# Kernel tuning notes

Hardware: AMD Instinct MI355X
Metric: run time of the kernel (lower is better)

The kernel has to match this reference:

```python
import jax, jax.numpy as jnp
import numpy as np
from jax.scipy.special import logsumexp

B, T, H, S = 32, 2000, 256, 63  # batch, time steps, hidden dim, num_states (=num_classes)


def setup_inputs() -> dict:
    key = jax.random.key(0)
    ks = jax.random.split(key, 5)
    return {
        "ctc_logits": jax.random.normal(ks[0], (B, T, S), dtype=jnp.float32),
        "frame_embeddings": jax.random.normal(ks[1], (B, T, H), dtype=jnp.float32),
        "keyword_tokens": jax.random.randint(ks[2], (B, 32), 0, S),
        "W1": jax.random.normal(ks[3], (2 * H, H), dtype=jnp.float32) * 0.02,
        "b1": jnp.zeros((H,), dtype=jnp.float32),
        "W2": jax.random.normal(ks[4], (H, S), dtype=jnp.float32) * 0.02,
        "b2": jnp.zeros((S,), dtype=jnp.float32),
    }


def reference(ctc_logits, frame_embeddings, keyword_tokens, W1, b1, W2, b2):
    Bv, Tv, Sv = ctc_logits.shape
    logp = jax.nn.log_softmax(ctc_logits, axis=-1)  # (B,T,S)

    # transition scores for frame pair (t, t-1) <-> trans_all[t-1], batched over all t at once
    pairs = jnp.concatenate([frame_embeddings[:, 1:], frame_embeddings[:, :-1]], axis=-1)  # (B,T-1,2H)
    h = jax.nn.relu(jnp.einsum("bti,ij->btj", pairs, W1) + b1)
    trans = jnp.einsum("bti,ij->btj", h, W2) + b2  # (B,T-1,S)

    lp_t = jnp.swapaxes(logp, 0, 1)   # (T,B,S)
    tr_t = jnp.swapaxes(trans, 0, 1)  # (T-1,B,S)

    # forward recursion
    f0 = jnp.zeros((Bv, Sv), dtype=logp.dtype).at[:, 0].set(
        logp[jnp.arange(Bv), 0, keyword_tokens[:, 0]])

    def fstep(f_prev, x):
        lp, tr = x  # each (B,S)
        # [b,j,s] = f_prev[b,j] + lp[b,s] + tr[b,s]; reduce over j (prev state)
        scores = f_prev[:, :, None] + lp[:, None, :] + tr[:, None, :]
        f = logsumexp(scores, axis=1)
        return f, f

    _, f_rest = jax.lax.scan(fstep, f0, (lp_t[1:], tr_t))
    fwd = jnp.concatenate([f0[None], f_rest], axis=0)  # (T,B,S)

    # backward recursion (reverse scan); backward at t uses pair (t+1, t) = trans[t]
    bT = jnp.zeros((Bv, Sv), dtype=logp.dtype)

    def bstep(b_next, x):
        lp, tr = x  # lp = logp[t+1], tr = trans[t]
        # [b,s,k] = b_next[b,k] + lp[b,s] + tr[b,s]; reduce over k (next state)
        scores = b_next[:, None, :] + lp[:, :, None] + tr[:, :, None]
        b = logsumexp(scores, axis=2)
        return b, b

    _, b_rest = jax.lax.scan(bstep, bT, (lp_t[1:], tr_t), reverse=True)
    bwd = jnp.concatenate([b_rest, bT[None]], axis=0)  # (T,B,S)

    alignments = jax.nn.softmax(jnp.swapaxes(fwd + bwd, 0, 1), axis=-1)  # (B,T,S)
    return alignments
```

## Files before the change

### kernel.cpp

```cpp
#include <hip/hip_runtime.h>
#include <stdint.h>

#define NB 32
#define NT 2000
#define NH 256
#define NS 63
#define LDSROW 264

typedef __attribute__((ext_vector_type(8))) short bf16x8;
typedef __attribute__((ext_vector_type(4))) float f32x4;

__device__ inline unsigned short f2bf(float f) {
  union { float f; uint32_t u; } v; v.f = f;
  return (unsigned short)((v.u + 0x7fffu + ((v.u >> 16) & 1u)) >> 16);
}
__device__ inline unsigned int pk2(float a, float b) {
  return (unsigned int)f2bf(a) | ((unsigned int)f2bf(b) << 16);
}
__device__ inline bf16x8 pack8(const float* g) {
  union { bf16x8 v; unsigned int u[4]; } c;
  c.u[0] = pk2(g[0], g[1]); c.u[1] = pk2(g[2], g[3]);
  c.u[2] = pk2(g[4], g[5]); c.u[3] = pk2(g[6], g[7]);
  return c.v;
}

#define NSLOT1 (16 * 4 * 4 * 64)
#define NSLOT2 (8 * 4 * 64)
#define WS_NEEDED ((size_t)(NSLOT1 + NSLOT2) * 16)

__global__ __launch_bounds__(256) void prep_weights(
    const float* __restrict__ W1, const float* __restrict__ W2,
    unsigned short* __restrict__ w1f, unsigned short* __restrict__ w2f) {
  const int tid = blockIdx.x * 256 + threadIdx.x;
  if (tid < NSLOT1) {
    const int lane = tid & 63;
    const int quad = lane >> 4, l16 = lane & 15;
    int r = tid >> 6;
    const int tn = r & 3; r >>= 2;
    const int wv = r & 3; r >>= 2;
    const int km = r;
    const int kb = (km >> 3) * 256 + (km & 7) * 32 + quad * 8;
    const int n = wv * 64 + tn * 16 + l16;
    ushort4 lo, hi;
    lo.x = f2bf(W1[(size_t)(kb + 0) * NH + n]);
    lo.y = f2bf(W1[(size_t)(kb + 1) * NH + n]);
    lo.z = f2bf(W1[(size_t)(kb + 2) * NH + n]);
    lo.w = f2bf(W1[(size_t)(kb + 3) * NH + n]);
    hi.x = f2bf(W1[(size_t)(kb + 4) * NH + n]);
    hi.y = f2bf(W1[(size_t)(kb + 5) * NH + n]);
    hi.z = f2bf(W1[(size_t)(kb + 6) * NH + n]);
    hi.w = f2bf(W1[(size_t)(kb + 7) * NH + n]);
    *(ushort4*)&w1f[(size_t)tid * 8] = lo;
    *(ushort4*)&w1f[(size_t)tid * 8 + 4] = hi;
  } else if (tid < NSLOT1 + NSLOT2) {
    const int t2 = tid - NSLOT1;
    const int lane = t2 & 63;
    const int quad = lane >> 4, l16 = lane & 15;
    const int tn = (t2 >> 6) & 3;
    const int ks = t2 >> 8;
    const int kb = ks * 32 + quad * 8;
    const int n = tn * 16 + l16;
    ushort4 lo = {0, 0, 0, 0}, hi = {0, 0, 0, 0};
    if (n < NS) {
      lo.x = f2bf(W2[(size_t)(kb + 0) * NS + n]);
      lo.y = f2bf(W2[(size_t)(kb + 1) * NS + n]);
      lo.z = f2bf(W2[(size_t)(kb + 2) * NS + n]);
      lo.w = f2bf(W2[(size_t)(kb + 3) * NS + n]);
      hi.x = f2bf(W2[(size_t)(kb + 4) * NS + n]);
      hi.y = f2bf(W2[(size_t)(kb + 5) * NS + n]);
      hi.z = f2bf(W2[(size_t)(kb + 6) * NS + n]);
      hi.w = f2bf(W2[(size_t)(kb + 7) * NS + n]);
    }
    *(ushort4*)&w2f[(size_t)t2 * 8] = lo;
    *(ushort4*)&w2f[(size_t)t2 * 8 + 4] = hi;
  }
}

template <bool PACKED>
__global__ __launch_bounds__(256, 4) void fused_kernel(
    const float* __restrict__ E, const float* __restrict__ logits,
    const int* __restrict__ kw,
    const float* __restrict__ W1, const float* __restrict__ W2,
    const unsigned short* __restrict__ w1f, const unsigned short* __restrict__ w2f,
    const float* __restrict__ b1, const float* __restrict__ b2,
    float* __restrict__ out) {
  const int b = blockIdx.y;
  const int a0 = blockIdx.x * 63;
  const int base = a0 - 1;
  const int tid = threadIdx.x;
  const int w = tid >> 6;
  const int lane = tid & 63;
  const int quad = lane >> 4;
  const int l16 = lane & 15;
  const int n0 = w * 64;

  __shared__ unsigned short lds[65 * LDSROW];
  float* TRf = (float*)lds;

  const float* Eb = E + (size_t)b * NT * NH;
  const float* lb = logits + (size_t)b * NT * NS;

  #pragma unroll
  for (int it = 0; it < 16; ++it) {
    const int row = it * 4 + w;
    int tr = base + row;
    tr = (tr < 0) ? 0 : (tr > NT - 1 ? NT - 1 : tr);
    float4 v = *(const float4*)&Eb[(size_t)tr * NH + (lane << 2)];
    ushort4 o;
    o.x = f2bf(v.x); o.y = f2bf(v.y); o.z = f2bf(v.z); o.w = f2bf(v.w);
    *(ushort4*)&lds[row * LDSROW + (lane << 2)] = o;
  }
  if (tid < 64) {
    int tr = base + 64; if (tr > NT - 1) tr = NT - 1;
    float4 v = *(const float4*)&Eb[(size_t)tr * NH + (lane << 2)];
    ushort4 o;
    o.x = f2bf(v.x); o.y = f2bf(v.y); o.z = f2bf(v.z); o.w = f2bf(v.w);
    *(ushort4*)&lds[64 * LDSROW + (lane << 2)] = o;
  }
  __syncthreads();

  f32x4 acc[4][4];
  #pragma unroll
  for (int tm = 0; tm < 4; ++tm)
    #pragma unroll
    for (int tn = 0; tn < 4; ++tn) acc[tm][tn] = (f32x4){0.f, 0.f, 0.f, 0.f};

  if constexpr (PACKED) {
    const unsigned short* wbase = w1f + (size_t)(((w << 2) * 64) + lane) * 8;
#define W1F_AT(KM, TN) \
  (*(const bf16x8*)(wbase + ((size_t)((((KM) << 4) + (TN))) << 9)))
    bf16x8 cb0 = W1F_AT(0, 0), cb1 = W1F_AT(0, 1);
    bf16x8 cb2 = W1F_AT(0, 2), cb3 = W1F_AT(0, 3);
    #pragma unroll
    for (int km = 0; km < 16; ++km) {
      bf16x8 nb0, nb1, nb2, nb3;
      if (km < 15) {
        nb0 = W1F_AT(km + 1, 0); nb1 = W1F_AT(km + 1, 1);
        nb2 = W1F_AT(km + 1, 2); nb3 = W1F_AT(km + 1, 3);
      }
      const int aoff = (km >> 3) ? 0 : 1;
      bf16x8 af[4];
      #pragma unroll
      for (int tm = 0; tm < 4; ++tm)
        af[tm] = *(const bf16x8*)&lds[(tm * 16 + l16 + aoff) * LDSROW +
                                      (km & 7) * 32 + quad * 8];
      #pragma unroll
      for (int tm = 0; tm < 4; ++tm)
        acc[tm][0] = __builtin_amdgcn_mfma_f32_16x16x32_bf16(af[tm], cb0, acc[tm][0], 0, 0, 0);
      #pragma unroll
      for (int tm = 0; tm < 4; ++tm)
        acc[tm][1] = __builtin_amdgcn_mfma_f32_16x16x32_bf16(af[tm], cb1, acc[tm][1], 0, 0, 0);
      #pragma unroll
      for (int tm = 0; tm < 4; ++tm)
        acc[tm][2] = __builtin_amdgcn_mfma_f32_16x16x32_bf16(af[tm], cb2, acc[tm][2], 0, 0, 0);
      #pragma unroll
      for (int tm = 0; tm < 4; ++tm)
        acc[tm][3] = __builtin_amdgcn_mfma_f32_16x16x32_bf16(af[tm], cb3, acc[tm][3], 0, 0, 0);
      if (km < 15) { cb0 = nb0; cb1 = nb1; cb2 = nb2; cb3 = nb3; }
    }
#undef W1F_AT
  } else {
    const float* w1p = W1 + (size_t)(quad * 8) * NH + n0 + l16;
    #pragma unroll
    for (int km = 0; km < 16; ++km) {
      const int hk = (km >> 3) * 256 + (km & 7) * 32;
      const int aoff = (km >> 3) ? 0 : 1;
      bf16x8 af[4];
      #pragma unroll
      for (int tm = 0; tm < 4; ++tm)
        af[tm] = *(const bf16x8*)&lds[(tm * 16 + l16 + aoff) * LDSROW +
                                      (km & 7) * 32 + quad * 8];
      float g[8], gn[8];
      #pragma unroll
      for (int j = 0; j < 8; ++j) g[j] = w1p[(size_t)(hk + j) * NH];
      #pragma unroll
      for (int tn = 0; tn < 4; ++tn) {
        if (tn < 3) {
          #pragma unroll
          for (int j = 0; j < 8; ++j)
            gn[j] = w1p[(size_t)(hk + j) * NH + (tn + 1) * 16];
        }
        bf16x8 bq = pack8(g);
        #pragma unroll
        for (int tm = 0; tm < 4; ++tm)
          acc[tm][tn] = __builtin_amdgcn_mfma_f32_16x16x32_bf16(
              af[tm], bq, acc[tm][tn], 0, 0, 0);
        if (tn < 3) {
          #pragma unroll
          for (int j = 0; j < 8; ++j) g[j] = gn[j];
        }
      }
    }
  }
  __syncthreads();

  #pragma unroll
  for (int tn = 0; tn < 4; ++tn) {
    float b1v = b1[n0 + tn * 16 + l16];
    #pragma unroll
    for (int tm = 0; tm < 4; ++tm)
      #pragma unroll
      for (int r = 0; r < 4; ++r) {
        float hv = fmaxf(acc[tm][tn][r] + b1v, 0.f);
        lds[(tm * 16 + quad * 4 + r) * LDSROW + n0 + tn * 16 + l16] = f2bf(hv);
      }
  }
  __syncthreads();

  const int m0 = w * 16;
  float lpv[16];
  #pragma unroll
  for (int tn = 0; tn < 4; ++tn) {
    const int s = tn * 16 + l16;
    const int cc = (s < NS) ? s : NS - 1;
    #pragma unroll
    for (int r = 0; r < 4; ++r) {
      int tt = a0 + m0 + quad * 4 + r;
      if (tt > NT - 1) tt = NT - 1;
      lpv[tn * 4 + r] = lb[(size_t)tt * NS + cc];
    }
  }

  f32x4 acc2[4];
  #pragma unroll
  for (int tn = 0; tn < 4; ++tn) acc2[tn] = (f32x4){0.f, 0.f, 0.f, 0.f};

  if constexpr (PACKED) {
    const unsigned short* w2base = w2f + (size_t)lane * 8;
    #pragma unroll
    for (int ks = 0; ks < 8; ++ks) {
      bf16x8 af = *(const bf16x8*)&lds[(m0 + l16) * LDSROW + ks * 32 + quad * 8];
      #pragma unroll
      for (int tn = 0; tn < 4; ++tn) {
        bf16x8 bq = *(const bf16x8*)(w2base + ((size_t)((ks << 2) + tn) << 9));
        acc2[tn] = __builtin_amdgcn_mfma_f32_16x16x32_bf16(af, bq, acc2[tn], 0, 0, 0);
      }
    }
  } else {
    #pragma unroll
    for (int ks = 0; ks < 8; ++ks) {
      const int k0 = ks * 32;
      bf16x8 af = *(const bf16x8*)&lds[(m0 + l16) * LDSROW + k0 + quad * 8];
      #pragma unroll
      for (int tn = 0; tn < 4; ++tn) {
        const int n = tn * 16 + l16;
        float g[8];
        #pragma unroll
        for (int j = 0; j < 8; ++j)
          g[j] = (n < NS) ? W2[(size_t)(k0 + quad * 8 + j) * NS + n] : 0.f;
        bf16x8 bq = pack8(g);
        acc2[tn] = __builtin_amdgcn_mfma_f32_16x16x32_bf16(af, bq, acc2[tn], 0, 0, 0);
      }
    }
  }
  __syncthreads();

  #pragma unroll
  for (int tn = 0; tn < 4; ++tn) {
    const int s = tn * 16 + l16;
    const float b2v = (s < NS) ? b2[s] : 0.f;
    #pragma unroll
    for (int r = 0; r < 4; ++r)
      TRf[(m0 + quad * 4 + r) * 68 + s] = acc2[tn][r] + b2v + lpv[tn * 4 + r];
  }
  __syncthreads();

  for (int rr = 0; rr < 16; ++rr) {
    const int j = m0 + rr;
    const int t = a0 + j;
    if (j == 63 || t > NT - 1) continue;
    float sc;
    if (t == 0) {
      float v = (lane < NS) ? lb[lane] : -1e30f;
      float m = v;
      #pragma unroll
      for (int o = 32; o > 0; o >>= 1) m = fmaxf(m, __shfl_xor(m, o));
      float ee = (lane < NS) ? __expf(v - m) : 0.f;
      float ss = ee;
      #pragma unroll
      for (int o = 32; o > 0; o >>= 1) ss += __shfl_xor(ss, o);
      const float lse = m + __logf(ss);
      const float f00 = lb[kw[b * 32]] - lse;
      sc = ((lane == 0) ? f00 : 0.f) + TRf[68 + lane];
    } else if (t == NT - 1) {
      sc = TRf[j * 68 + lane];
    } else {
      sc = TRf[j * 68 + lane] + TRf[(j + 1) * 68 + lane];
    }
    float e = (lane < NS) ? __expf(sc) : 0.f;
    float s = e;
    #pragma unroll
    for (int o = 32; o > 0; o >>= 1) s += __shfl_xor(s, o);
    if (lane < NS) out[((size_t)b * NT + t) * NS + lane] = e / s;
  }
}

extern "C" void kernel_launch(void* const* d_in, const int* in_sizes, int n_in,
                              void* d_out, int out_size, void* d_ws, size_t ws_size,
                              hipStream_t stream) {
  const float* logits = (const float*)d_in[0];
  const float* E      = (const float*)d_in[1];
  const int*   kw     = (const int*)d_in[2];
  const float* W1     = (const float*)d_in[3];
  const float* b1     = (const float*)d_in[4];
  const float* W2     = (const float*)d_in[5];
  const float* b2     = (const float*)d_in[6];
  float* out = (float*)d_out;

  dim3 g(32, NB);

  if (ws_size >= WS_NEEDED && d_ws != nullptr) {
    unsigned short* w1f = (unsigned short*)d_ws;
    unsigned short* w2f = w1f + (size_t)NSLOT1 * 8;
    prep_weights<<<dim3((NSLOT1 + NSLOT2) / 256), 256, 0, stream>>>(W1, W2, w1f, w2f);
    fused_kernel<true><<<g, 256, 0, stream>>>(E, logits, kw, W1, W2, w1f, w2f,
                                              b1, b2, out);
  } else {
    fused_kernel<false><<<g, 256, 0, stream>>>(E, logits, kw, W1, W2, nullptr,
                                               nullptr, b1, b2, out);
  }
}
```

Baseline: 139.9 us.

## Process two time tiles per block with register-prefetched second tile overlapping GEMM

Each block now handles two consecutive 63-frame tiles instead of one, halving the grid. The second tile's embedding rows are loaded into registers while the first tile's first GEMM runs, and its first GEMM overlaps the first tile's softmax store, using a second LDS buffer. The intent is to hide global load latency behind MFMA work. In exchange it uses double the LDS, lowers launch bounds to 2 blocks per CU and holds 17 extra float4 registers, which cuts occupancy and the number of blocks available to fill the GPU.

```diff
diff --git a/kernel.cpp b/kernel.cpp
--- a/kernel.cpp
+++ b/kernel.cpp
@@ -6,6 +6,7 @@
 #define NH 256
 #define NS 63
 #define LDSROW 264
+#define TILE_USHORTS (65 * LDSROW)
 
 typedef __attribute__((ext_vector_type(8))) short bf16x8;
 typedef __attribute__((ext_vector_type(4))) float f32x4;
@@ -76,30 +77,10 @@
   }
 }
 
-template <bool PACKED>
-__global__ __launch_bounds__(256, 4) void fused_kernel(
-    const float* __restrict__ E, const float* __restrict__ logits,
-    const int* __restrict__ kw,
-    const float* __restrict__ W1, const float* __restrict__ W2,
-    const unsigned short* __restrict__ w1f, const unsigned short* __restrict__ w2f,
-    const float* __restrict__ b1, const float* __restrict__ b2,
-    float* __restrict__ out) {
-  const int b = blockIdx.y;
-  const int a0 = blockIdx.x * 63;
-  const int base = a0 - 1;
-  const int tid = threadIdx.x;
-  const int w = tid >> 6;
-  const int lane = tid & 63;
-  const int quad = lane >> 4;
-  const int l16 = lane & 15;
-  const int n0 = w * 64;
-
-  __shared__ unsigned short lds[65 * LDSROW];
-  float* TRf = (float*)lds;
-
-  const float* Eb = E + (size_t)b * NT * NH;
-  const float* lb = logits + (size_t)b * NT * NS;
-
+
+__device__ __forceinline__ void stage_direct(const float* __restrict__ Eb,
+                                             unsigned short* R, int base,
+                                             int tid, int w, int lane) {
   #pragma unroll
   for (int it = 0; it < 16; ++it) {
     const int row = it * 4 + w;
@@ -108,92 +89,131 @@
     float4 v = *(const float4*)&Eb[(size_t)tr * NH + (lane << 2)];
     ushort4 o;
     o.x = f2bf(v.x); o.y = f2bf(v.y); o.z = f2bf(v.z); o.w = f2bf(v.w);
-    *(ushort4*)&lds[row * LDSROW + (lane << 2)] = o;
+    *(ushort4*)&R[row * LDSROW + (lane << 2)] = o;
   }
   if (tid < 64) {
     int tr = base + 64; if (tr > NT - 1) tr = NT - 1;
     float4 v = *(const float4*)&Eb[(size_t)tr * NH + (lane << 2)];
     ushort4 o;
     o.x = f2bf(v.x); o.y = f2bf(v.y); o.z = f2bf(v.z); o.w = f2bf(v.w);
-    *(ushort4*)&lds[64 * LDSROW + (lane << 2)] = o;
-  }
-  __syncthreads();
-
-  f32x4 acc[4][4];
-  #pragma unroll
-  for (int tm = 0; tm < 4; ++tm)
-    #pragma unroll
-    for (int tn = 0; tn < 4; ++tn) acc[tm][tn] = (f32x4){0.f, 0.f, 0.f, 0.f};
-
-  if constexpr (PACKED) {
-    const unsigned short* wbase = w1f + (size_t)(((w << 2) * 64) + lane) * 8;
-#define W1F_AT(KM, TN) \
-  (*(const bf16x8*)(wbase + ((size_t)((((KM) << 4) + (TN))) << 9)))
-    bf16x8 cb0 = W1F_AT(0, 0), cb1 = W1F_AT(0, 1);
-    bf16x8 cb2 = W1F_AT(0, 2), cb3 = W1F_AT(0, 3);
-    #pragma unroll
-    for (int km = 0; km < 16; ++km) {
-      bf16x8 nb0, nb1, nb2, nb3;
-      if (km < 15) {
-        nb0 = W1F_AT(km + 1, 0); nb1 = W1F_AT(km + 1, 1);
-        nb2 = W1F_AT(km + 1, 2); nb3 = W1F_AT(km + 1, 3);
+    *(ushort4*)&R[64 * LDSROW + (lane << 2)] = o;
+  }
+}
+
+__device__ __forceinline__ void prefetch_rows(const float* __restrict__ Eb,
+                                              int base, int tid, int w, int lane,
+                                              float4 eb[17]) {
+  #pragma unroll
+  for (int it = 0; it < 16; ++it) {
+    const int row = it * 4 + w;
+    int tr = base + row;
+    tr = (tr < 0) ? 0 : (tr > NT - 1 ? NT - 1 : tr);
+    eb[it] = *(const float4*)&Eb[(size_t)tr * NH + (lane << 2)];
+  }
+  if (tid < 64) {
+    int tr = base + 64; if (tr > NT - 1) tr = NT - 1;
+    eb[16] = *(const float4*)&Eb[(size_t)tr * NH + (lane << 2)];
+  }
+}
+
+__device__ __forceinline__ void write_rows(unsigned short* R, int tid, int w,
+                                           int lane, const float4 eb[17]) {
+  #pragma unroll
+  for (int it = 0; it < 16; ++it) {
+    const int row = it * 4 + w;
+    float4 v = eb[it];
+    ushort4 o;
+    o.x = f2bf(v.x); o.y = f2bf(v.y); o.z = f2bf(v.z); o.w = f2bf(v.w);
+    *(ushort4*)&R[row * LDSROW + (lane << 2)] = o;
+  }
+  if (tid < 64) {
+    float4 v = eb[16];
+    ushort4 o;
+    o.x = f2bf(v.x); o.y = f2bf(v.y); o.z = f2bf(v.z); o.w = f2bf(v.w);
+    *(ushort4*)&R[64 * LDSROW + (lane << 2)] = o;
+  }
+}
+
+__device__ __forceinline__ void gemm1_packed(
+    const unsigned short* R, const unsigned short* __restrict__ w1f,
+    int w, int lane, int quad, int l16, f32x4 acc[4][4]) {
+  const unsigned short* wbase = w1f + (size_t)(((w << 2) * 64) + lane) * 8;
+  bf16x8 cb0 = *(const bf16x8*)(wbase + ((size_t)0 << 9));
+  bf16x8 cb1 = *(const bf16x8*)(wbase + ((size_t)1 << 9));
+  bf16x8 cb2 = *(const bf16x8*)(wbase + ((size_t)2 << 9));
+  bf16x8 cb3 = *(const bf16x8*)(wbase + ((size_t)3 << 9));
+  #pragma unroll
+  for (int km = 0; km < 16; ++km) {
+    bf16x8 nb0, nb1, nb2, nb3;
+    if (km < 15) {
+      nb0 = *(const bf16x8*)(wbase + ((size_t)(((km + 1) << 4) + 0) << 9));
+      nb1 = *(const bf16x8*)(wbase + ((size_t)(((km + 1) << 4) + 1) << 9));
+      nb2 = *(const bf16x8*)(wbase + ((size_t)(((km + 1) << 4) + 2) << 9));
+      nb3 = *(const bf16x8*)(wbase + ((size_t)(((km + 1) << 4) + 3) << 9));
+    }
+    const int aoff = (km >> 3) ? 0 : 1;
+    bf16x8 af[4];
+    #pragma unroll
+    for (int tm = 0; tm < 4; ++tm)
+      af[tm] = *(const bf16x8*)&R[(tm * 16 + l16 + aoff) * LDSROW +
+                                  (km & 7) * 32 + quad * 8];
+    #pragma unroll
+    for (int tm = 0; tm < 4; ++tm)
+      acc[tm][0] = __builtin_amdgcn_mfma_f32_16x16x32_bf16(af[tm], cb0, acc[tm][0], 0, 0, 0);
+    #pragma unroll
+    for (int tm = 0; tm < 4; ++tm)
+      acc[tm][1] = __builtin_amdgcn_mfma_f32_16x16x32_bf16(af[tm], cb1, acc[tm][1], 0, 0, 0);
+    #pragma unroll
+    for (int tm = 0; tm < 4; ++tm)
+      acc[tm][2] = __builtin_amdgcn_mfma_f32_16x16x32_bf16(af[tm], cb2, acc[tm][2], 0, 0, 0);
+    #pragma unroll
+    for (int tm = 0; tm < 4; ++tm)
+      acc[tm][3] = __builtin_amdgcn_mfma_f32_16x16x32_bf16(af[tm], cb3, acc[tm][3], 0, 0, 0);
+    if (km < 15) { cb0 = nb0; cb1 = nb1; cb2 = nb2; cb3 = nb3; }
+  }
+}
+
+__device__ __forceinline__ void gemm1_gather(
+    const unsigned short* R, const float* __restrict__ W1,
+    int w, int lane, int quad, int l16, f32x4 acc[4][4]) {
+  const int n0 = w * 64;
+  const float* w1p = W1 + (size_t)(quad * 8) * NH + n0 + l16;
+  #pragma unroll
+  for (int km = 0; km < 16; ++km) {
+    const int hk = (km >> 3) * 256 + (km & 7) * 32;
+    const int aoff = (km >> 3) ? 0 : 1;
+    bf16x8 af[4];
+    #pragma unroll
+    for (int tm = 0; tm < 4; ++tm)
+      af[tm] = *(const bf16x8*)&R[(tm * 16 + l16 + aoff) * LDSROW +
+                                  (km & 7) * 32 + quad * 8];
+    float g[8], gn[8];
+    #pragma unroll
+    for (int j = 0; j < 8; ++j) g[j] = w1p[(size_t)(hk + j) * NH];
+    #pragma unroll
+    for (int tn = 0; tn < 4; ++tn) {
+      if (tn < 3) {
+        #pragma unroll
+        for (int j = 0; j < 8; ++j)
+          gn[j] = w1p[(size_t)(hk + j) * NH + (tn + 1) * 16];
       }
-      const int aoff = (km >> 3) ? 0 : 1;
-      bf16x8 af[4];
+      bf16x8 bq = pack8(g);
       #pragma unroll
       for (int tm = 0; tm < 4; ++tm)
-        af[tm] = *(const bf16x8*)&lds[(tm * 16 + l16 + aoff) * LDSROW +
-                                      (km & 7) * 32 + quad * 8];
-      #pragma unroll
-      for (int tm = 0; tm < 4; ++tm)
-        acc[tm][0] = __builtin_amdgcn_mfma_f32_16x16x32_bf16(af[tm], cb0, acc[tm][0], 0, 0, 0);
-      #pragma unroll
-      for (int tm = 0; tm < 4; ++tm)
-        acc[tm][1] = __builtin_amdgcn_mfma_f32_16x16x32_bf16(af[tm], cb1, acc[tm][1], 0, 0, 0);
-      #pragma unroll
-      for (int tm = 0; tm < 4; ++tm)
-        acc[tm][2] = __builtin_amdgcn_mfma_f32_16x16x32_bf16(af[tm], cb2, acc[tm][2], 0, 0, 0);
-      #pragma unroll
-      for (int tm = 0; tm < 4; ++tm)
-        acc[tm][3] = __builtin_amdgcn_mfma_f32_16x16x32_bf16(af[tm], cb3, acc[tm][3], 0, 0, 0);
-      if (km < 15) { cb0 = nb0; cb1 = nb1; cb2 = nb2; cb3 = nb3; }
-    }
-#undef W1F_AT
-  } else {
-    const float* w1p = W1 + (size_t)(quad * 8) * NH + n0 + l16;
-    #pragma unroll
-    for (int km = 0; km < 16; ++km) {
-      const int hk = (km >> 3) * 256 + (km & 7) * 32;
-      const int aoff = (km >> 3) ? 0 : 1;
-      bf16x8 af[4];
-      #pragma unroll
-      for (int tm = 0; tm < 4; ++tm)
-        af[tm] = *(const bf16x8*)&lds[(tm * 16 + l16 + aoff) * LDSROW +
-                                      (km & 7) * 32 + quad * 8];
-      float g[8], gn[8];
-      #pragma unroll
-      for (int j = 0; j < 8; ++j) g[j] = w1p[(size_t)(hk + j) * NH];
-      #pragma unroll
-      for (int tn = 0; tn < 4; ++tn) {
-        if (tn < 3) {
-          #pragma unroll
-          for (int j = 0; j < 8; ++j)
-            gn[j] = w1p[(size_t)(hk + j) * NH + (tn + 1) * 16];
-        }
-        bf16x8 bq = pack8(g);
+        acc[tm][tn] = __builtin_amdgcn_mfma_f32_16x16x32_bf16(
+            af[tm], bq, acc[tm][tn], 0, 0, 0);
+      if (tn < 3) {
         #pragma unroll
-        for (int tm = 0; tm < 4; ++tm)
-          acc[tm][tn] = __builtin_amdgcn_mfma_f32_16x16x32_bf16(
-              af[tm], bq, acc[tm][tn], 0, 0, 0);
-        if (tn < 3) {
-          #pragma unroll
-          for (int j = 0; j < 8; ++j) g[j] = gn[j];
-        }
+        for (int j = 0; j < 8; ++j) g[j] = gn[j];
       }
     }
   }
-  __syncthreads();
-
+}
+
+__device__ __forceinline__ void write_h(unsigned short* R, const float* __restrict__ b1,
+                                        int w, int quad, int l16,
+                                        const f32x4 acc[4][4]) {
+  const int n0 = w * 64;
   #pragma unroll
   for (int tn = 0; tn < 4; ++tn) {
     float b1v = b1[n0 + tn * 16 + l16];
@@ -202,13 +222,14 @@
       #pragma unroll
       for (int r = 0; r < 4; ++r) {
         float hv = fmaxf(acc[tm][tn][r] + b1v, 0.f);
-        lds[(tm * 16 + quad * 4 + r) * LDSROW + n0 + tn * 16 + l16] = f2bf(hv);
+        R[(tm * 16 + quad * 4 + r) * LDSROW + n0 + tn * 16 + l16] = f2bf(hv);
       }
   }
-  __syncthreads();
-
-  const int m0 = w * 16;
-  float lpv[16];
+}
+
+__device__ __forceinline__ void prefetch_lpv(const float* __restrict__ lb,
+                                             int a0, int m0, int quad, int l16,
+                                             float lpv[16]) {
   #pragma unroll
   for (int tn = 0; tn < 4; ++tn) {
     const int s = tn * 16 + l16;
@@ -220,41 +241,48 @@
       lpv[tn * 4 + r] = lb[(size_t)tt * NS + cc];
     }
   }
-
-  f32x4 acc2[4];
-  #pragma unroll
-  for (int tn = 0; tn < 4; ++tn) acc2[tn] = (f32x4){0.f, 0.f, 0.f, 0.f};
-
-  if constexpr (PACKED) {
-    const unsigned short* w2base = w2f + (size_t)lane * 8;
-    #pragma unroll
-    for (int ks = 0; ks < 8; ++ks) {
-      bf16x8 af = *(const bf16x8*)&lds[(m0 + l16) * LDSROW + ks * 32 + quad * 8];
+}
+
+__device__ __forceinline__ void gemm2_packed(
+    const unsigned short* R, const unsigned short* __restrict__ w2f,
+    int w, int lane, int quad, int l16, f32x4 acc2[4]) {
+  const int m0 = w * 16;
+  const unsigned short* w2base = w2f + (size_t)lane * 8;
+  #pragma unroll
+  for (int ks = 0; ks < 8; ++ks) {
+    bf16x8 af = *(const bf16x8*)&R[(m0 + l16) * LDSROW + ks * 32 + quad * 8];
+    #pragma unroll
+    for (int tn = 0; tn < 4; ++tn) {
+      bf16x8 bq = *(const bf16x8*)(w2base + ((size_t)((ks << 2) + tn) << 9));
+      acc2[tn] = __builtin_amdgcn_mfma_f32_16x16x32_bf16(af, bq, acc2[tn], 0, 0, 0);
+    }
+  }
+}
+
+__device__ __forceinline__ void gemm2_gather(
+    const unsigned short* R, const float* __restrict__ W2,
+    int w, int lane, int quad, int l16, f32x4 acc2[4]) {
+  const int m0 = w * 16;
+  #pragma unroll
+  for (int ks = 0; ks < 8; ++ks) {
+    const int k0 = ks * 32;
+    bf16x8 af = *(const bf16x8*)&R[(m0 + l16) * LDSROW + k0 + quad * 8];
+    #pragma unroll
+    for (int tn = 0; tn < 4; ++tn) {
+      const int n = tn * 16 + l16;
+      float g[8];
       #pragma unroll
-      for (int tn = 0; tn < 4; ++tn) {
-        bf16x8 bq = *(const bf16x8*)(w2base + ((size_t)((ks << 2) + tn) << 9));
-        acc2[tn] = __builtin_amdgcn_mfma_f32_16x16x32_bf16(af, bq, acc2[tn], 0, 0, 0);
-      }
-    }
-  } else {
-    #pragma unroll
-    for (int ks = 0; ks < 8; ++ks) {
-      const int k0 = ks * 32;
-      bf16x8 af = *(const bf16x8*)&lds[(m0 + l16) * LDSROW + k0 + quad * 8];
-      #pragma unroll
-      for (int tn = 0; tn < 4; ++tn) {
-        const int n = tn * 16 + l16;
-        float g[8];
-        #pragma unroll
-        for (int j = 0; j < 8; ++j)
-          g[j] = (n < NS) ? W2[(size_t)(k0 + quad * 8 + j) * NS + n] : 0.f;
-        bf16x8 bq = pack8(g);
-        acc2[tn] = __builtin_amdgcn_mfma_f32_16x16x32_bf16(af, bq, acc2[tn], 0, 0, 0);
-      }
-    }
-  }
-  __syncthreads();
-
+      for (int j = 0; j < 8; ++j)
+        g[j] = (n < NS) ? W2[(size_t)(k0 + quad * 8 + j) * NS + n] : 0.f;
+      bf16x8 bq = pack8(g);
+      acc2[tn] = __builtin_amdgcn_mfma_f32_16x16x32_bf16(af, bq, acc2[tn], 0, 0, 0);
+    }
+  }
+}
+
+__device__ __forceinline__ void write_U(float* TRf, const float* __restrict__ b2,
+                                        const float lpv[16], int m0, int quad,
+                                        int l16, const f32x4 acc2[4]) {
   #pragma unroll
   for (int tn = 0; tn < 4; ++tn) {
     const int s = tn * 16 + l16;
@@ -263,8 +291,11 @@
     for (int r = 0; r < 4; ++r)
       TRf[(m0 + quad * 4 + r) * 68 + s] = acc2[tn][r] + b2v + lpv[tn * 4 + r];
   }
-  __syncthreads();
-
+}
+
+__device__ __forceinline__ void softmax_store(const float* TRf,
+    const float* __restrict__ lb, const int* __restrict__ kw,
+    float* __restrict__ out, int b, int a0, int m0, int lane) {
   for (int rr = 0; rr < 16; ++rr) {
     const int j = m0 + rr;
     const int t = a0 + j;
@@ -295,6 +326,89 @@
   }
 }
 
+template <bool PACKED>
+__global__ __launch_bounds__(256, 2) void fused_kernel(
+    const float* __restrict__ E, const float* __restrict__ logits,
+    const int* __restrict__ kw,
+    const float* __restrict__ W1, const float* __restrict__ W2,
+    const unsigned short* __restrict__ w1f, const unsigned short* __restrict__ w2f,
+    const float* __restrict__ b1, const float* __restrict__ b2,
+    float* __restrict__ out) {
+  const int b = blockIdx.y;
+  const int a0A = blockIdx.x * 126;
+  const int a0B = a0A + 63;
+  const int tid = threadIdx.x;
+  const int w = tid >> 6;
+  const int lane = tid & 63;
+  const int quad = lane >> 4;
+  const int l16 = lane & 15;
+  const int m0 = w * 16;
+
+  extern __shared__ unsigned short lds[];
+  unsigned short* R1 = lds;
+  unsigned short* R2 = lds + TILE_USHORTS;
+  float* TRf = (float*)lds;
+
+  const float* Eb = E + (size_t)b * NT * NH;
+  const float* lb = logits + (size_t)b * NT * NS;
+
+  stage_direct(Eb, R1, a0A - 1, tid, w, lane);
+  __syncthreads();
+
+  float4 eb[17];
+  prefetch_rows(Eb, a0B - 1, tid, w, lane, eb);
+
+  f32x4 acc[4][4];
+  #pragma unroll
+  for (int tm = 0; tm < 4; ++tm)
+    #pragma unroll
+    for (int tn = 0; tn < 4; ++tn) acc[tm][tn] = (f32x4){0.f, 0.f, 0.f, 0.f};
+  if constexpr (PACKED) gemm1_packed(R1, w1f, w, lane, quad, l16, acc);
+  else                  gemm1_gather(R1, W1, w, lane, quad, l16, acc);
+  __syncthreads();
+
+  write_rows(R2, tid, w, lane, eb);
+  write_h(R1, b1, w, quad, l16, acc);
+  __syncthreads();
+
+  float lpvA[16];
+  prefetch_lpv(lb, a0A, m0, quad, l16, lpvA);
+  f32x4 acc2[4];
+  #pragma unroll
+  for (int tn = 0; tn < 4; ++tn) acc2[tn] = (f32x4){0.f, 0.f, 0.f, 0.f};
+  if constexpr (PACKED) gemm2_packed(R1, w2f, w, lane, quad, l16, acc2);
+  else                  gemm2_gather(R1, W2, w, lane, quad, l16, acc2);
+  __syncthreads();
+
+  write_U(TRf, b2, lpvA, m0, quad, l16, acc2);
+  __syncthreads();
+
+  float lpvB[16];
+  prefetch_lpv(lb, a0B, m0, quad, l16, lpvB);
+  #pragma unroll
+  for (int tm = 0; tm < 4; ++tm)
+    #pragma unroll
+    for (int tn = 0; tn < 4; ++tn) acc[tm][tn] = (f32x4){0.f, 0.f, 0.f, 0.f};
+  if constexpr (PACKED) gemm1_packed(R2, w1f, w, lane, quad, l16, acc);
+  else                  gemm1_gather(R2, W1, w, lane, quad, l16, acc);
+  softmax_store(TRf, lb, kw, out, b, a0A, m0, lane);
+  __syncthreads();
+
+  write_h(R1, b1, w, quad, l16, acc);
+  __syncthreads();
+
+  #pragma unroll
+  for (int tn = 0; tn < 4; ++tn) acc2[tn] = (f32x4){0.f, 0.f, 0.f, 0.f};
+  if constexpr (PACKED) gemm2_packed(R1, w2f, w, lane, quad, l16, acc2);
+  else                  gemm2_gather(R1, W2, w, lane, quad, l16, acc2);
+  __syncthreads();
+
+  write_U(TRf, b2, lpvB, m0, quad, l16, acc2);
+  __syncthreads();
+
+  softmax_store(TRf, lb, kw, out, b, a0B, m0, lane);
+}
+
 extern "C" void kernel_launch(void* const* d_in, const int* in_sizes, int n_in,
                               void* d_out, int out_size, void* d_ws, size_t ws_size,
                               hipStream_t stream) {
@@ -307,16 +421,17 @@
   const float* b2     = (const float*)d_in[6];
   float* out = (float*)d_out;
 
-  dim3 g(32, NB);
+  dim3 g(16, NB);
+  const size_t shmem = (size_t)2 * TILE_USHORTS * sizeof(unsigned short);
 
   if (ws_size >= WS_NEEDED && d_ws != nullptr) {
     unsigned short* w1f = (unsigned short*)d_ws;
     unsigned short* w2f = w1f + (size_t)NSLOT1 * 8;
     prep_weights<<<dim3((NSLOT1 + NSLOT2) / 256), 256, 0, stream>>>(W1, W2, w1f, w2f);
-    fused_kernel<true><<<g, 256, 0, stream>>>(E, logits, kw, W1, W2, w1f, w2f,
-                                              b1, b2, out);
+    fused_kernel<true><<<g, 256, shmem, stream>>>(E, logits, kw, W1, W2, w1f, w2f,
+                                                  b1, b2, out);
   } else {
-    fused_kernel<false><<<g, 256, 0, stream>>>(E, logits, kw, W1, W2, nullptr,
-                                               nullptr, b1, b2, out);
-  }
-}
+    fused_kernel<false><<<g, 256, shmem, stream>>>(E, logits, kw, W1, W2, nullptr,
+                                                   nullptr, b1, b2, out);
+  }
+}
```

Measured after the change: 155.4 us. +11.0%, slower.
